# Performance work log

Measured on AMD Instinct MI355X. Metric: run time of the kernel, lower is better.

The kernel has to match this reference:

```python
import jax, jax.numpy as jnp
import numpy as np

WINDOW_SIZES = (5, 10, 20)
EPS = 1e-5


def setup_inputs() -> dict:
    key = jax.random.key(0)
    x = jax.random.normal(key, (32, 4096, 128), dtype=jnp.float32)
    weights = jnp.ones((len(WINDOW_SIZES),), dtype=jnp.float32)
    return {"x": x, "weights": weights}


def _sliding_center_norm(x, w, eps):
    # x: (B, L, F). Normalize each length-w window (biased var), keep only the
    # center element of each window, then zero-pad back to length L.
    B, L, F = x.shape
    c = w // 2
    n = L - w + 1  # number of windows
    zp = jnp.zeros((B, 1, F), x.dtype)
    cs = jnp.concatenate([zp, jnp.cumsum(x, axis=1)], axis=1)        # (B, L+1, F)
    cs2 = jnp.concatenate([zp, jnp.cumsum(x * x, axis=1)], axis=1)   # (B, L+1, F)
    mean = (cs[:, w:] - cs[:, :n]) / w                                # (B, n, F)
    m2 = (cs2[:, w:] - cs2[:, :n]) / w
    var = jnp.maximum(m2 - mean * mean, 0.0)  # biased var (unbiased=False)
    std = jnp.sqrt(var + eps)
    center = x[:, c:c + n]  # element at center index of each window
    normed = (center - mean) / std
    pad_right = L - n - c
    return jnp.pad(normed, ((0, 0), (c, pad_right), (0, 0)))


def reference(x, weights):
    x = jnp.nan_to_num(x, nan=0.0, posinf=0.0, neginf=0.0)
    w_soft = jax.nn.softmax(weights, axis=0)
    out = jnp.zeros_like(x)
    for i, w in enumerate(WINDOW_SIZES):
        out = out + w_soft[i] * _sliding_center_norm(x, w, EPS)
    return out
```

## Files before the change

### kernel.cpp

```cpp
#include <hip/hip_runtime.h>
#include <math.h>

#pragma clang fp contract(off)

#define LL 4096
#define FF 128
#define NB 32
#define BASE 16
#define NBLK 256
#define NOB 16

__device__ __forceinline__ float sani(float v) {
    return (fabsf(v) <= 3.0e38f) ? v : 0.0f;
}

__global__ __launch_bounds__(256) void k_tiles(const float* __restrict__ x,
                                               float2* __restrict__ T0) {
    const int pair = (int)blockIdx.x;
    const int b    = (int)blockIdx.y;
    const int tid  = (int)threadIdx.x;
    const int f    = tid & 127;
    const int tile = pair * 2 + (tid >> 7);
    const float* xb = x + ((size_t)b * LL + (size_t)tile * 16) * FF + f;
    float cs, cs2;
    {
        const float v = sani(xb[0]);
        cs = v; cs2 = __fmul_rn(v, v);
    }
#pragma unroll
    for (int u = 1; u < 16; ++u) {
        const float v = sani(xb[(size_t)u * FF]);
        cs  = __fadd_rn(cs,  v);
        cs2 = __fadd_rn(cs2, __fmul_rn(v, v));
    }
    T0[((size_t)b * NBLK + tile) * FF + f] = make_float2(cs, cs2);
}

__global__ __launch_bounds__(128) void k_pref_a(float2* __restrict__ T0) {
    const int g = (int)blockIdx.x & 15;
    const int b = (int)blockIdx.x >> 4;
    const int f = (int)threadIdx.x;
    float2* p = T0 + ((size_t)b * NBLK + (size_t)g * 16) * FF + f;
    float2 t[16];
#pragma unroll
    for (int i = 0; i < 16; ++i) t[i] = p[(size_t)i * FF];
    float sx = t[0].x, sy = t[0].y;
#pragma unroll
    for (int i = 1; i < 16; ++i) {
        sx = __fadd_rn(sx, t[i].x);
        sy = __fadd_rn(sy, t[i].y);
        p[(size_t)i * FF] = make_float2(sx, sy);
    }
}

__global__ __launch_bounds__(128) void k_pref_b(const float2* __restrict__ S1,
                                                float2* __restrict__ S2) {
    const int b = (int)blockIdx.x;
    const int f = (int)threadIdx.x;
    const float2* base = S1 + (size_t)b * NBLK * FF + f;
    float2* s2 = S2 + (size_t)b * NOB * FF + f;
    float2 t = base[(size_t)15 * FF];
    float sx = t.x, sy = t.y;
    s2[0] = t;
    for (int g = 1; g < NOB; ++g) {
        const float2 tg = base[(size_t)(g * 16 + 15) * FF];
        sx = __fadd_rn(sx, tg.x);
        sy = __fadd_rn(sy, tg.y);
        s2[(size_t)g * FF] = make_float2(sx, sy);
    }
}

__global__ __launch_bounds__(256) void k_win2(const float* __restrict__ x,
                                              const float* __restrict__ w,
                                              const float2* __restrict__ S1,
                                              const float2* __restrict__ S2,
                                              float* __restrict__ out) {
    __shared__ float xs[64 * FF];
    const int pair = (int)blockIdx.x;
    const int b    = (int)blockIdx.y;
    const int tid  = (int)threadIdx.x;
    const int l0   = pair * 32 - 16;

    const float* xb = x + (size_t)b * LL * FF;
#pragma unroll
    for (int it = 0; it < 8; ++it) {
        const int idx = it * 1024 + tid * 4;
        const int row = idx >> 7;
        const int col = idx & 127;
        const int g   = l0 + row;
        float4 v = make_float4(0.0f, 0.0f, 0.0f, 0.0f);
        if ((unsigned)g < (unsigned)LL)
            v = *reinterpret_cast<const float4*>(xb + (size_t)g * FF + col);
        v.x = sani(v.x); v.y = sani(v.y); v.z = sani(v.z); v.w = sani(v.w);
        *reinterpret_cast<float4*>(&xs[row * FF + col]) = v;
    }
    __syncthreads();

    const int t    = tid >> 7;
    const int f    = tid & 127;
    const int tile = pair * 2 + t;
    const int rb   = t * 16;

    auto PB = [&](int B) -> float2 {
        if (B < 0) return make_float2(0.0f, 0.0f);
        float2 p = S1[((size_t)b * NBLK + B) * FF + f];
        const int g = B >> 4;
        if (g > 0) {
            const float2 s2 = S2[((size_t)b * NOB + (g - 1)) * FF + f];
            p.x = __fadd_rn(p.x, s2.x);
            p.y = __fadd_rn(p.y, s2.y);
        }
        return p;
    };
    const float2 PA  = PB(tile - 2);
    const float2 PBm = PB(tile - 1);
    const float2 PC  = PB(tile);

    float Vx[41], Vy[41], xr[16];

#define SEG(P0, N, PP, SAVE)                                         \
    {                                                                \
        float cs = 0.0f, cs2 = 0.0f;                                 \
        _Pragma("unroll")                                            \
        for (int u = 0; u < (N); ++u) {                              \
            const float v = xs[(rb + (P0) + u) * FF + f];            \
            if (SAVE) xr[u] = v;                                     \
            if (u == 0) { cs = v; cs2 = __fmul_rn(v, v); }           \
            else { cs = __fadd_rn(cs, v);                            \
                   cs2 = __fadd_rn(cs2, __fmul_rn(v, v)); }          \
            Vx[(P0) + u] = __fadd_rn(cs,  (PP).x);                   \
            Vy[(P0) + u] = __fadd_rn(cs2, (PP).y);                   \
        }                                                            \
    }
    SEG(0,  16, PA,  false)
    SEG(16, 16, PBm, true)
    SEG(32, 9,  PC,  false)
#undef SEG

    const float w0 = w[0], w1 = w[1], w2 = w[2];
    const float mx = fmaxf(w0, fmaxf(w1, w2));
    const float e0 = expf(w0 - mx), e1 = expf(w1 - mx), e2 = expf(w2 - mx);
    const float s  = e0 + e1 + e2;
    const float ws0 = e0 / s, ws1 = e1 / s, ws2 = e2 / s;

    float* ob = out + ((size_t)b * LL + (size_t)tile * 16) * FF + f;

#pragma unroll
    for (int u = 0; u < 16; ++u) {
        const int l = tile * 16 + u;
        const float xc = xr[u];
        const float g5  = (l >= 2  && l <= LL - 3)  ? ws0 : 0.0f;
        const float g10 = (l >= 5  && l <= LL - 5)  ? ws1 : 0.0f;
        const float g20 = (l >= 10 && l <= LL - 10) ? ws2 : 0.0f;
        float o;
        {
            const float mean = (Vx[u + 18] - Vx[u + 13]) * 0.2f;
            const float m2   = (Vy[u + 18] - Vy[u + 13]) * 0.2f;
            const float var  = fmaxf(m2 - mean * mean, 0.0f);
            o = g5 * ((xc - mean) * rsqrtf(var + 1e-5f));
        }
        {
            const float mean = (Vx[u + 20] - Vx[u + 10]) * 0.1f;
            const float m2   = (Vy[u + 20] - Vy[u + 10]) * 0.1f;
            const float var  = fmaxf(m2 - mean * mean, 0.0f);
            o += g10 * ((xc - mean) * rsqrtf(var + 1e-5f));
        }
        {
            const float mean = (Vx[u + 25] - Vx[u + 5]) * 0.05f;
            const float m2   = (Vy[u + 25] - Vy[u + 5]) * 0.05f;
            const float var  = fmaxf(m2 - mean * mean, 0.0f);
            o += g20 * ((xc - mean) * rsqrtf(var + 1e-5f));
        }
        ob[(size_t)u * FF] = o;
    }
}

__global__ __launch_bounds__(256) void fan_blocked(const float* __restrict__ x,
                                                   const float* __restrict__ w,
                                                   float* __restrict__ out) {
    __shared__ float2 V[LL];
    __shared__ float2 T0s[NBLK];
    __shared__ float2 T1[NOB];
    __shared__ float2 S2[NOB];
    const int col = blockIdx.x;
    const int f   = col & (FF - 1);
    const int b   = col >> 7;
    const int tid = (int)threadIdx.x;
    const float* xcol = x   + (size_t)b * LL * FF + f;
    float*       ocol = out + (size_t)b * LL * FF + f;
    for (int l = tid; l < LL; l += 256) {
        const float v = sani(xcol[(size_t)l * FF]);
        V[l] = make_float2(v, __fmul_rn(v, v));
    }
    __syncthreads();
    {
        const int bse = tid * BASE;
        float cs = V[bse].x, cs2 = V[bse].y;
        for (int u = 1; u < BASE; ++u) {
            const float2 e = V[bse + u];
            cs = __fadd_rn(cs, e.x); cs2 = __fadd_rn(cs2, e.y);
            V[bse + u] = make_float2(cs, cs2);
        }
        T0s[tid] = make_float2(cs, cs2);
    }
    __syncthreads();
    if (tid < NOB) {
        const int bse = tid * BASE;
        float cs = T0s[bse].x, cs2 = T0s[bse].y;
        for (int u = 1; u < BASE; ++u) {
            const float2 e = T0s[bse + u];
            cs = __fadd_rn(cs, e.x); cs2 = __fadd_rn(cs2, e.y);
            T0s[bse + u] = make_float2(cs, cs2);
        }
        T1[tid] = make_float2(cs, cs2);
    }
    __syncthreads();
    if (tid == 0) {
        float cs = T1[0].x, cs2 = T1[0].y;
        S2[0] = T1[0];
        for (int o = 1; o < NOB; ++o) {
            cs = __fadd_rn(cs, T1[o].x); cs2 = __fadd_rn(cs2, T1[o].y);
            S2[o] = make_float2(cs, cs2);
        }
    }
    __syncthreads();
    {
        const int blk = tid;
        if (blk > 0) {
            const int B = blk - 1, ob2 = B >> 4;
            float2 Pp = T0s[B];
            if (ob2 > 0) {
                const float2 s2 = S2[ob2 - 1];
                Pp = make_float2(__fadd_rn(Pp.x, s2.x), __fadd_rn(Pp.y, s2.y));
            }
            const int bse = blk * BASE;
            for (int u = 0; u < BASE; ++u) {
                const float2 sv = V[bse + u];
                V[bse + u] = make_float2(__fadd_rn(sv.x, Pp.x), __fadd_rn(sv.y, Pp.y));
            }
        }
    }
    __syncthreads();
    const float w0 = w[0], w1 = w[1], w2 = w[2];
    const float mx = fmaxf(w0, fmaxf(w1, w2));
    const float e0 = expf(w0 - mx), e1 = expf(w1 - mx), e2 = expf(w2 - mx);
    const float s  = e0 + e1 + e2;
    const float ws0 = e0 / s, ws1 = e1 / s, ws2 = e2 / s;
    auto PV = [&](int j) -> float2 {
        if (j <= 0) return make_float2(0.0f, 0.0f);
        int idx = j - 1; if (idx > LL - 1) idx = LL - 1;
        return V[idx];
    };
    for (int l = tid; l < LL; l += 256) {
        const float xc = sani(xcol[(size_t)l * FF]);
        const float2 A5 = PV(l + 3), B5 = PV(l - 2);
        const float2 A10 = PV(l + 5), B10 = PV(l - 5);
        const float2 A20 = PV(l + 10), B20 = PV(l - 10);
        const float g5  = (l >= 2  && l <= LL - 3)  ? ws0 : 0.0f;
        const float g10 = (l >= 5  && l <= LL - 5)  ? ws1 : 0.0f;
        const float g20 = (l >= 10 && l <= LL - 10) ? ws2 : 0.0f;
        float o;
        {
            const float mean = (A5.x - B5.x) * 0.2f;
            const float m2   = (A5.y - B5.y) * 0.2f;
            const float var  = fmaxf(m2 - mean * mean, 0.0f);
            o = g5 * ((xc - mean) * rsqrtf(var + 1e-5f));
        }
        {
            const float mean = (A10.x - B10.x) * 0.1f;
            const float m2   = (A10.y - B10.y) * 0.1f;
            const float var  = fmaxf(m2 - mean * mean, 0.0f);
            o += g10 * ((xc - mean) * rsqrtf(var + 1e-5f));
        }
        {
            const float mean = (A20.x - B20.x) * 0.05f;
            const float m2   = (A20.y - B20.y) * 0.05f;
            const float var  = fmaxf(m2 - mean * mean, 0.0f);
            o += g20 * ((xc - mean) * rsqrtf(var + 1e-5f));
        }
        ocol[(size_t)l * FF] = o;
    }
}

extern "C" void kernel_launch(void* const* d_in, const int* in_sizes, int n_in,
                              void* d_out, int out_size, void* d_ws, size_t ws_size,
                              hipStream_t stream) {
    const float* x = (const float*)d_in[0];
    const float* w = (const float*)d_in[1];
    float* out     = (float*)d_out;

    const size_t t0_bytes = (size_t)NB * NBLK * FF * sizeof(float2);
    if (ws_size >= 2 * t0_bytes) {
        float2* T0 = (float2*)d_ws;
        float2* S2 = (float2*)((char*)d_ws + t0_bytes);
        k_tiles <<<dim3(128, NB), dim3(256), 0, stream>>>(x, T0);
        k_pref_a<<<dim3(NB * 16), dim3(128), 0, stream>>>(T0);
        k_pref_b<<<dim3(NB),      dim3(128), 0, stream>>>(T0, S2);
        k_win2  <<<dim3(128, NB), dim3(256), 0, stream>>>(x, w, T0, S2, out);
    } else {
        fan_blocked<<<dim3(NB * FF), dim3(256), 0, stream>>>(x, w, out);
    }
}
```

Baseline: 64.70 us.

## Drop LDS staging in window kernel; process two features per thread with float2 loads

The final window kernel no longer stages a 64-row slab in shared memory behind a barrier. Each thread now loads its 41 rows directly from global memory as float2, handling two adjacent features with packed vector arithmetic. Each block covers four tiles, so the grid is halved, and a guard-free template path serves interior tiles. This removes LDS traffic and the __syncthreads, at the cost of more register pressure (two 41-entry float2 arrays) and redundant overlapping global reads that rely on cache.

```diff
diff --git a/kernel.cpp b/kernel.cpp
--- a/kernel.cpp
+++ b/kernel.cpp
@@ -9,6 +9,8 @@
 #define BASE 16
 #define NBLK 256
 #define NOB 16
+
+typedef float v2f __attribute__((ext_vector_type(2)));
 
 __device__ __forceinline__ float sani(float v) {
     return (fabsf(v) <= 3.0e38f) ? v : 0.0f;
@@ -70,72 +72,109 @@
     }
 }
 
-__global__ __launch_bounds__(256) void k_win2(const float* __restrict__ x,
+__device__ __forceinline__ void compose_P(const float2* __restrict__ S1,
+                                          const float2* __restrict__ S2,
+                                          int b, int B, int f,
+                                          v2f& pc, v2f& pq) {
+    pc = (v2f)0.0f; pq = (v2f)0.0f;
+    if (B < 0) return;
+    const float4 q = *reinterpret_cast<const float4*>(S1 + ((size_t)b * NBLK + B) * FF + f);
+    float c0 = q.x, q0 = q.y, c1 = q.z, q1 = q.w;
+    const int g = B >> 4;
+    if (g > 0) {
+        const float4 s2 = *reinterpret_cast<const float4*>(S2 + ((size_t)b * NOB + (g - 1)) * FF + f);
+        c0 = __fadd_rn(c0, s2.x); q0 = __fadd_rn(q0, s2.y);
+        c1 = __fadd_rn(c1, s2.z); q1 = __fadd_rn(q1, s2.w);
+    }
+    pc.x = c0; pc.y = c1; pq.x = q0; pq.y = q1;
+}
+
+template<bool GUARD>
+__device__ __forceinline__ void win_body3(const float* __restrict__ xb,
+                                          float* __restrict__ ob,
+                                          const int base, const int lbase,
+                                          const v2f PAc, const v2f PAq,
+                                          const v2f PBc, const v2f PBq,
+                                          const v2f PCc, const v2f PCq,
+                                          const float ws0, const float ws1, const float ws2) {
+    v2f Vx[41], Vy[41], xr[16];
+
+#define SEG(P0, N, PC_, PQ_, SAVE)                                        \
+    {                                                                     \
+        v2f cs = (v2f)0.0f, cs2 = (v2f)0.0f;                              \
+        _Pragma("unroll")                                                 \
+        for (int u = 0; u < (N); ++u) {                                   \
+            const int p = (P0) + u;                                       \
+            v2f v = (v2f)0.0f;                                            \
+            if (!GUARD || ((unsigned)(base + p) < (unsigned)LL)) {        \
+                const float2 t = *reinterpret_cast<const float2*>(        \
+                    xb + (p - 16) * FF);                                  \
+                v.x = sani(t.x); v.y = sani(t.y);                         \
+            }                                                             \
+            if (SAVE) xr[u] = v;                                          \
+            const v2f vq = v * v;                                         \
+            if (u == 0) { cs = v; cs2 = vq; }                             \
+            else        { cs = cs + v; cs2 = cs2 + vq; }                  \
+            Vx[p] = cs + (PC_);                                           \
+            Vy[p] = cs2 + (PQ_);                                          \
+        }                                                                 \
+    }
+    SEG(0,  16, PAc, PAq, false)
+    SEG(16, 16, PBc, PBq, true)
+    SEG(32, 9,  PCc, PCq, false)
+#undef SEG
+
+#pragma unroll
+    for (int u = 0; u < 16; ++u) {
+        const int l = lbase + u;
+        const v2f xc = xr[u];
+        const float g5  = (l >= 2  && l <= LL - 3)  ? ws0 : 0.0f;
+        const float g10 = (l >= 5  && l <= LL - 5)  ? ws1 : 0.0f;
+        const float g20 = (l >= 10 && l <= LL - 10) ? ws2 : 0.0f;
+        v2f o;
+        {
+            const v2f mean = (Vx[u + 18] - Vx[u + 13]) * 0.2f;
+            const v2f m2   = (Vy[u + 18] - Vy[u + 13]) * 0.2f;
+            const v2f var  = m2 - mean * mean;
+            v2f inv;
+            inv.x = rsqrtf(fmaxf(var.x, 0.0f) + 1e-5f);
+            inv.y = rsqrtf(fmaxf(var.y, 0.0f) + 1e-5f);
+            o = ((xc - mean) * inv) * g5;
+        }
+        {
+            const v2f mean = (Vx[u + 20] - Vx[u + 10]) * 0.1f;
+            const v2f m2   = (Vy[u + 20] - Vy[u + 10]) * 0.1f;
+            const v2f var  = m2 - mean * mean;
+            v2f inv;
+            inv.x = rsqrtf(fmaxf(var.x, 0.0f) + 1e-5f);
+            inv.y = rsqrtf(fmaxf(var.y, 0.0f) + 1e-5f);
+            o = o + ((xc - mean) * inv) * g10;
+        }
+        {
+            const v2f mean = (Vx[u + 25] - Vx[u + 5]) * 0.05f;
+            const v2f m2   = (Vy[u + 25] - Vy[u + 5]) * 0.05f;
+            const v2f var  = m2 - mean * mean;
+            v2f inv;
+            inv.x = rsqrtf(fmaxf(var.x, 0.0f) + 1e-5f);
+            inv.y = rsqrtf(fmaxf(var.y, 0.0f) + 1e-5f);
+            o = o + ((xc - mean) * inv) * g20;
+        }
+        *reinterpret_cast<float2*>(ob + (size_t)u * FF) = make_float2(o.x, o.y);
+    }
+}
+
+__global__ __launch_bounds__(256) void k_win3(const float* __restrict__ x,
                                               const float* __restrict__ w,
                                               const float2* __restrict__ S1,
                                               const float2* __restrict__ S2,
                                               float* __restrict__ out) {
-    __shared__ float xs[64 * FF];
-    const int pair = (int)blockIdx.x;
-    const int b    = (int)blockIdx.y;
-    const int tid  = (int)threadIdx.x;
-    const int l0   = pair * 32 - 16;
-
-    const float* xb = x + (size_t)b * LL * FF;
-#pragma unroll
-    for (int it = 0; it < 8; ++it) {
-        const int idx = it * 1024 + tid * 4;
-        const int row = idx >> 7;
-        const int col = idx & 127;
-        const int g   = l0 + row;
-        float4 v = make_float4(0.0f, 0.0f, 0.0f, 0.0f);
-        if ((unsigned)g < (unsigned)LL)
-            v = *reinterpret_cast<const float4*>(xb + (size_t)g * FF + col);
-        v.x = sani(v.x); v.y = sani(v.y); v.z = sani(v.z); v.w = sani(v.w);
-        *reinterpret_cast<float4*>(&xs[row * FF + col]) = v;
-    }
-    __syncthreads();
-
-    const int t    = tid >> 7;
-    const int f    = tid & 127;
-    const int tile = pair * 2 + t;
-    const int rb   = t * 16;
-
-    auto PB = [&](int B) -> float2 {
-        if (B < 0) return make_float2(0.0f, 0.0f);
-        float2 p = S1[((size_t)b * NBLK + B) * FF + f];
-        const int g = B >> 4;
-        if (g > 0) {
-            const float2 s2 = S2[((size_t)b * NOB + (g - 1)) * FF + f];
-            p.x = __fadd_rn(p.x, s2.x);
-            p.y = __fadd_rn(p.y, s2.y);
-        }
-        return p;
-    };
-    const float2 PA  = PB(tile - 2);
-    const float2 PBm = PB(tile - 1);
-    const float2 PC  = PB(tile);
-
-    float Vx[41], Vy[41], xr[16];
-
-#define SEG(P0, N, PP, SAVE)                                         \
-    {                                                                \
-        float cs = 0.0f, cs2 = 0.0f;                                 \
-        _Pragma("unroll")                                            \
-        for (int u = 0; u < (N); ++u) {                              \
-            const float v = xs[(rb + (P0) + u) * FF + f];            \
-            if (SAVE) xr[u] = v;                                     \
-            if (u == 0) { cs = v; cs2 = __fmul_rn(v, v); }           \
-            else { cs = __fadd_rn(cs, v);                            \
-                   cs2 = __fadd_rn(cs2, __fmul_rn(v, v)); }          \
-            Vx[(P0) + u] = __fadd_rn(cs,  (PP).x);                   \
-            Vy[(P0) + u] = __fadd_rn(cs2, (PP).y);                   \
-        }                                                            \
-    }
-    SEG(0,  16, PA,  false)
-    SEG(16, 16, PBm, true)
-    SEG(32, 9,  PC,  false)
-#undef SEG
+    const int qb  = (int)blockIdx.x;
+    const int b   = (int)blockIdx.y;
+    const int tid = (int)threadIdx.x;
+    const int tile = qb * 4 + (tid >> 6);
+    const int f    = (tid & 63) * 2;
+    const int lbase = tile * 16;
+    const int base  = lbase - 16;
 
     const float w0 = w[0], w1 = w[1], w2 = w[2];
     const float mx = fmaxf(w0, fmaxf(w1, w2));
@@ -143,36 +182,18 @@
     const float s  = e0 + e1 + e2;
     const float ws0 = e0 / s, ws1 = e1 / s, ws2 = e2 / s;
 
-    float* ob = out + ((size_t)b * LL + (size_t)tile * 16) * FF + f;
-
-#pragma unroll
-    for (int u = 0; u < 16; ++u) {
-        const int l = tile * 16 + u;
-        const float xc = xr[u];
-        const float g5  = (l >= 2  && l <= LL - 3)  ? ws0 : 0.0f;
-        const float g10 = (l >= 5  && l <= LL - 5)  ? ws1 : 0.0f;
-        const float g20 = (l >= 10 && l <= LL - 10) ? ws2 : 0.0f;
-        float o;
-        {
-            const float mean = (Vx[u + 18] - Vx[u + 13]) * 0.2f;
-            const float m2   = (Vy[u + 18] - Vy[u + 13]) * 0.2f;
-            const float var  = fmaxf(m2 - mean * mean, 0.0f);
-            o = g5 * ((xc - mean) * rsqrtf(var + 1e-5f));
-        }
-        {
-            const float mean = (Vx[u + 20] - Vx[u + 10]) * 0.1f;
-            const float m2   = (Vy[u + 20] - Vy[u + 10]) * 0.1f;
-            const float var  = fmaxf(m2 - mean * mean, 0.0f);
-            o += g10 * ((xc - mean) * rsqrtf(var + 1e-5f));
-        }
-        {
-            const float mean = (Vx[u + 25] - Vx[u + 5]) * 0.05f;
-            const float m2   = (Vy[u + 25] - Vy[u + 5]) * 0.05f;
-            const float var  = fmaxf(m2 - mean * mean, 0.0f);
-            o += g20 * ((xc - mean) * rsqrtf(var + 1e-5f));
-        }
-        ob[(size_t)u * FF] = o;
-    }
+    v2f PAc, PAq, PBc, PBq, PCc, PCq;
+    compose_P(S1, S2, b, tile - 2, f, PAc, PAq);
+    compose_P(S1, S2, b, tile - 1, f, PBc, PBq);
+    compose_P(S1, S2, b, tile,     f, PCc, PCq);
+
+    const float* xb = x   + ((size_t)b * LL + lbase) * FF + f;
+    float*       ob = out + ((size_t)b * LL + lbase) * FF + f;
+
+    if (tile >= 1 && tile <= NBLK - 2)
+        win_body3<false>(xb, ob, base, lbase, PAc, PAq, PBc, PBq, PCc, PCq, ws0, ws1, ws2);
+    else
+        win_body3<true >(xb, ob, base, lbase, PAc, PAq, PBc, PBq, PCc, PCq, ws0, ws1, ws2);
 }
 
 __global__ __launch_bounds__(256) void fan_blocked(const float* __restrict__ x,
@@ -296,7 +317,7 @@
         k_tiles <<<dim3(128, NB), dim3(256), 0, stream>>>(x, T0);
         k_pref_a<<<dim3(NB * 16), dim3(128), 0, stream>>>(T0);
         k_pref_b<<<dim3(NB),      dim3(128), 0, stream>>>(T0, S2);
-        k_win2  <<<dim3(128, NB), dim3(256), 0, stream>>>(x, w, T0, S2, out);
+        k_win3  <<<dim3(64, NB),  dim3(256), 0, stream>>>(x, w, T0, S2, out);
     } else {
         fan_blocked<<<dim3(NB * FF), dim3(256), 0, stream>>>(x, w, out);
     }
```

New measurement: 69.09 us. +6.8%, slower.

## Share halo prefix sums between paired tiles via LDS instead of staging x

Applied to the files above, without the earlier changes.

The window kernel no longer stages a 64-row slab of x in shared memory. Each half-block now reads its own 32 (or 25) rows of x straight from global memory, builds running prefix sums, and passes the boundary prefix values to its sibling half through small shared arrays with one barrier. This cuts the x rows read per block from 64 to about 57, shrinks LDS use, and removes bounds checks on interior blocks through a templated guard. In exchange, loads become column-strided scalar reads rather than float4 loads, and the two halves now do uneven work.

```diff
diff --git a/kernel.cpp b/kernel.cpp
--- a/kernel.cpp
+++ b/kernel.cpp
@@ -70,72 +70,135 @@
     }
 }
 
-__global__ __launch_bounds__(256) void k_win2(const float* __restrict__ x,
+__device__ __forceinline__ float2 PB_load(const float2* __restrict__ S1,
+                                          const float2* __restrict__ S2,
+                                          int b, int B, int f) {
+    if (B < 0) return make_float2(0.0f, 0.0f);
+    float2 p = S1[((size_t)b * NBLK + B) * FF + f];
+    const int g = B >> 4;
+    if (g > 0) {
+        const float2 s2 = S2[((size_t)b * NOB + (g - 1)) * FF + f];
+        p.x = __fadd_rn(p.x, s2.x);
+        p.y = __fadd_rn(p.y, s2.y);
+    }
+    return p;
+}
+
+template<bool GUARD>
+__device__ __forceinline__ void win4_body(const float* __restrict__ xcolB,
+                                          float* __restrict__ out,
+                                          const float2* __restrict__ S1,
+                                          const float2* __restrict__ S2,
+                                          int b, int f, int t, int pair,
+                                          float* __restrict__ Ax, float* __restrict__ Ay,
+                                          float* __restrict__ Bx, float* __restrict__ By,
+                                          float ws0, float ws1, float ws2) {
+    const int tileO = pair * 2 + t;
+
+    float VPx[16], VPy[16], VOx[16], VOy[16], VNx[9], VNy[9], xr[16];
+
+#define CHAINN(N, r0, PP, Cx, Cy, SAVEXR)                                \
+    {                                                                    \
+        float cs = 0.0f, cs2 = 0.0f;                                     \
+        _Pragma("unroll")                                                \
+        for (int u = 0; u < (N); ++u) {                                  \
+            float v = 0.0f;                                              \
+            if (!GUARD || ((unsigned)((r0) + u) < (unsigned)LL))         \
+                v = sani(xcolB[(size_t)((r0) + u) * FF]);                \
+            if (SAVEXR) xr[u] = v;                                       \
+            if (u == 0) { cs = v; cs2 = __fmul_rn(v, v); }               \
+            else { cs = __fadd_rn(cs, v);                                \
+                   cs2 = __fadd_rn(cs2, __fmul_rn(v, v)); }              \
+            Cx[u] = __fadd_rn(cs,  (PP).x);                              \
+            Cy[u] = __fadd_rn(cs2, (PP).y);                              \
+        }                                                                \
+    }
+
+    if (t == 0) {
+        const float2 PH = PB_load(S1, S2, b, tileO - 2, f);
+        const float2 PO = PB_load(S1, S2, b, tileO - 1, f);
+        CHAINN(16, (tileO - 1) * 16, PH, VPx, VPy, false)
+        CHAINN(16, tileO * 16,       PO, VOx, VOy, true)
+#pragma unroll
+        for (int i = 5; i < 16; ++i) {
+            Ax[(i - 5) * FF + f] = VOx[i];
+            Ay[(i - 5) * FF + f] = VOy[i];
+        }
+    } else {
+        const float2 PO = PB_load(S1, S2, b, tileO - 1, f);
+        float2 PN = make_float2(0.0f, 0.0f);
+        if (!GUARD || (tileO + 1 <= NBLK - 1))
+            PN = PB_load(S1, S2, b, tileO, f);
+        CHAINN(16, tileO * 16,       PO, VOx, VOy, true)
+        CHAINN(9,  (tileO + 1) * 16, PN, VNx, VNy, false)
+#pragma unroll
+        for (int i = 0; i < 9; ++i) {
+            Bx[i * FF + f] = VOx[i];
+            By[i * FF + f] = VOy[i];
+        }
+    }
+    __syncthreads();
+    if (t == 0) {
+#pragma unroll
+        for (int i = 0; i < 9; ++i) { VNx[i] = Bx[i * FF + f]; VNy[i] = By[i * FF + f]; }
+    } else {
+#pragma unroll
+        for (int i = 5; i < 16; ++i) { VPx[i] = Ax[(i - 5) * FF + f]; VPy[i] = Ay[(i - 5) * FF + f]; }
+    }
+#undef CHAINN
+
+    auto GX = [&](int p) -> float {
+        return p < 16 ? VPx[p] : (p < 32 ? VOx[p - 16] : VNx[p - 32]);
+    };
+    auto GY = [&](int p) -> float {
+        return p < 16 ? VPy[p] : (p < 32 ? VOy[p - 16] : VNy[p - 32]);
+    };
+
+    const int lbase = tileO * 16;
+    float* ob = out + (size_t)lbase * FF;
+
+#pragma unroll
+    for (int u = 0; u < 16; ++u) {
+        const int l = lbase + u;
+        const float xc = xr[u];
+        const float g5  = (l >= 2  && l <= LL - 3)  ? ws0 : 0.0f;
+        const float g10 = (l >= 5  && l <= LL - 5)  ? ws1 : 0.0f;
+        const float g20 = (l >= 10 && l <= LL - 10) ? ws2 : 0.0f;
+        float o;
+        {
+            const float mean = (GX(u + 18) - GX(u + 13)) * 0.2f;
+            const float m2   = (GY(u + 18) - GY(u + 13)) * 0.2f;
+            const float var  = fmaxf(m2 - mean * mean, 0.0f);
+            o = g5 * ((xc - mean) * rsqrtf(var + 1e-5f));
+        }
+        {
+            const float mean = (GX(u + 20) - GX(u + 10)) * 0.1f;
+            const float m2   = (GY(u + 20) - GY(u + 10)) * 0.1f;
+            const float var  = fmaxf(m2 - mean * mean, 0.0f);
+            o += g10 * ((xc - mean) * rsqrtf(var + 1e-5f));
+        }
+        {
+            const float mean = (GX(u + 25) - GX(u + 5)) * 0.05f;
+            const float m2   = (GY(u + 25) - GY(u + 5)) * 0.05f;
+            const float var  = fmaxf(m2 - mean * mean, 0.0f);
+            o += g20 * ((xc - mean) * rsqrtf(var + 1e-5f));
+        }
+        ob[(size_t)u * FF] = o;
+    }
+}
+
+__global__ __launch_bounds__(256) void k_win4(const float* __restrict__ x,
                                               const float* __restrict__ w,
                                               const float2* __restrict__ S1,
                                               const float2* __restrict__ S2,
                                               float* __restrict__ out) {
-    __shared__ float xs[64 * FF];
+    __shared__ float Ax[11 * FF], Ay[11 * FF];
+    __shared__ float Bx[9 * FF],  By[9 * FF];
     const int pair = (int)blockIdx.x;
     const int b    = (int)blockIdx.y;
     const int tid  = (int)threadIdx.x;
-    const int l0   = pair * 32 - 16;
-
-    const float* xb = x + (size_t)b * LL * FF;
-#pragma unroll
-    for (int it = 0; it < 8; ++it) {
-        const int idx = it * 1024 + tid * 4;
-        const int row = idx >> 7;
-        const int col = idx & 127;
-        const int g   = l0 + row;
-        float4 v = make_float4(0.0f, 0.0f, 0.0f, 0.0f);
-        if ((unsigned)g < (unsigned)LL)
-            v = *reinterpret_cast<const float4*>(xb + (size_t)g * FF + col);
-        v.x = sani(v.x); v.y = sani(v.y); v.z = sani(v.z); v.w = sani(v.w);
-        *reinterpret_cast<float4*>(&xs[row * FF + col]) = v;
-    }
-    __syncthreads();
-
     const int t    = tid >> 7;
     const int f    = tid & 127;
-    const int tile = pair * 2 + t;
-    const int rb   = t * 16;
-
-    auto PB = [&](int B) -> float2 {
-        if (B < 0) return make_float2(0.0f, 0.0f);
-        float2 p = S1[((size_t)b * NBLK + B) * FF + f];
-        const int g = B >> 4;
-        if (g > 0) {
-            const float2 s2 = S2[((size_t)b * NOB + (g - 1)) * FF + f];
-            p.x = __fadd_rn(p.x, s2.x);
-            p.y = __fadd_rn(p.y, s2.y);
-        }
-        return p;
-    };
-    const float2 PA  = PB(tile - 2);
-    const float2 PBm = PB(tile - 1);
-    const float2 PC  = PB(tile);
-
-    float Vx[41], Vy[41], xr[16];
-
-#define SEG(P0, N, PP, SAVE)                                         \
-    {                                                                \
-        float cs = 0.0f, cs2 = 0.0f;                                 \
-        _Pragma("unroll")                                            \
-        for (int u = 0; u < (N); ++u) {                              \
-            const float v = xs[(rb + (P0) + u) * FF + f];            \
-            if (SAVE) xr[u] = v;                                     \
-            if (u == 0) { cs = v; cs2 = __fmul_rn(v, v); }           \
-            else { cs = __fadd_rn(cs, v);                            \
-                   cs2 = __fadd_rn(cs2, __fmul_rn(v, v)); }          \
-            Vx[(P0) + u] = __fadd_rn(cs,  (PP).x);                   \
-            Vy[(P0) + u] = __fadd_rn(cs2, (PP).y);                   \
-        }                                                            \
-    }
-    SEG(0,  16, PA,  false)
-    SEG(16, 16, PBm, true)
-    SEG(32, 9,  PC,  false)
-#undef SEG
 
     const float w0 = w[0], w1 = w[1], w2 = w[2];
     const float mx = fmaxf(w0, fmaxf(w1, w2));
@@ -143,36 +206,13 @@
     const float s  = e0 + e1 + e2;
     const float ws0 = e0 / s, ws1 = e1 / s, ws2 = e2 / s;
 
-    float* ob = out + ((size_t)b * LL + (size_t)tile * 16) * FF + f;
-
-#pragma unroll
-    for (int u = 0; u < 16; ++u) {
-        const int l = tile * 16 + u;
-        const float xc = xr[u];
-        const float g5  = (l >= 2  && l <= LL - 3)  ? ws0 : 0.0f;
-        const float g10 = (l >= 5  && l <= LL - 5)  ? ws1 : 0.0f;
-        const float g20 = (l >= 10 && l <= LL - 10) ? ws2 : 0.0f;
-        float o;
-        {
-            const float mean = (Vx[u + 18] - Vx[u + 13]) * 0.2f;
-            const float m2   = (Vy[u + 18] - Vy[u + 13]) * 0.2f;
-            const float var  = fmaxf(m2 - mean * mean, 0.0f);
-            o = g5 * ((xc - mean) * rsqrtf(var + 1e-5f));
-        }
-        {
-            const float mean = (Vx[u + 20] - Vx[u + 10]) * 0.1f;
-            const float m2   = (Vy[u + 20] - Vy[u + 10]) * 0.1f;
-            const float var  = fmaxf(m2 - mean * mean, 0.0f);
-            o += g10 * ((xc - mean) * rsqrtf(var + 1e-5f));
-        }
-        {
-            const float mean = (Vx[u + 25] - Vx[u + 5]) * 0.05f;
-            const float m2   = (Vy[u + 25] - Vy[u + 5]) * 0.05f;
-            const float var  = fmaxf(m2 - mean * mean, 0.0f);
-            o += g20 * ((xc - mean) * rsqrtf(var + 1e-5f));
-        }
-        ob[(size_t)u * FF] = o;
-    }
+    const float* xcolB = x   + (size_t)b * LL * FF + f;
+    float*       ocol  = out + (size_t)b * LL * FF + f;
+
+    if (pair >= 1 && pair <= 126)
+        win4_body<false>(xcolB, ocol, S1, S2, b, f, t, pair, Ax, Ay, Bx, By, ws0, ws1, ws2);
+    else
+        win4_body<true >(xcolB, ocol, S1, S2, b, f, t, pair, Ax, Ay, Bx, By, ws0, ws1, ws2);
 }
 
 __global__ __launch_bounds__(256) void fan_blocked(const float* __restrict__ x,
@@ -296,7 +336,7 @@
         k_tiles <<<dim3(128, NB), dim3(256), 0, stream>>>(x, T0);
         k_pref_a<<<dim3(NB * 16), dim3(128), 0, stream>>>(T0);
         k_pref_b<<<dim3(NB),      dim3(128), 0, stream>>>(T0, S2);
-        k_win2  <<<dim3(128, NB), dim3(256), 0, stream>>>(x, w, T0, S2, out);
+        k_win4  <<<dim3(128, NB), dim3(256), 0, stream>>>(x, w, T0, S2, out);
     } else {
         fan_blocked<<<dim3(NB * FF), dim3(256), 0, stream>>>(x, w, out);
     }
```

Result: slower. 72.38 us (+11.9%).
